# Kernel tuning notes

Measured on AMD Instinct MI355X. Metric: run time of the kernel, lower is better.

Reference implementation:

```python
import jax, jax.numpy as jnp
import numpy as np

N = 50000      # nodes
E = 800000     # edges (avg degree 16)
D = 64         # embedding_dim
G = 64         # graphs in batch
V = 30         # node label vocab (hard-coded in module)


def setup_inputs() -> dict:
    key = jax.random.key(0)
    ks = jax.random.split(key, 12)
    x = jax.random.randint(ks[0], (N,), 0, V, dtype=jnp.int32)
    edge_index = jax.random.randint(ks[1], (2, E), 0, N, dtype=jnp.int32)
    edge_attr = jax.random.uniform(ks[2], (E,), dtype=jnp.float32)
    batch = jnp.sort(jax.random.randint(ks[3], (N,), 0, G, dtype=jnp.int32))
    emb = jax.random.normal(ks[4], (V, D), dtype=jnp.float32)
    s = 1.0 / np.sqrt(D)
    W1 = jax.random.uniform(ks[5], (D, D), jnp.float32, -s, s)
    b1 = jnp.zeros((D,), jnp.float32)
    W2 = jax.random.uniform(ks[6], (D, D), jnp.float32, -s, s)
    b2 = jnp.zeros((D,), jnp.float32)
    W3 = jax.random.uniform(ks[7], (D, D), jnp.float32, -s, s)
    b3 = jnp.zeros((D,), jnp.float32)
    return {"x": x, "edge_index": edge_index, "edge_attr": edge_attr,
            "batch": batch, "emb": emb, "W1": W1, "b1": b1,
            "W2": W2, "b2": b2, "W3": W3, "b3": b3}


def _gcn(h, W, b, src, dst, norm, inv_deg):
    # GCNConv with self-loops: out_i = sum_{j->i} norm_ij * (h_j W) + (1/deg_i) * (h_i W) + b
    h = h @ W
    agg = jax.ops.segment_sum(h[src] * norm[:, None], dst, num_segments=N)
    return agg + h * inv_deg[:, None] + b


def reference(x, edge_index, edge_attr, batch, emb, W1, b1, W2, b2, W3, b3):
    src, dst = edge_index[0], edge_index[1]
    # symmetric GCN normalization with self-loops (weight 1)
    deg = jax.ops.segment_sum(edge_attr, dst, num_segments=N) + 1.0
    dis = deg ** -0.5                      # deg >= 1, so finite
    norm = dis[src] * edge_attr * dis[dst]
    inv_deg = 1.0 / deg                    # self-loop norm = dis_i * 1 * dis_i

    h = emb[x]                             # [N, D]
    h = jax.nn.relu(_gcn(h, W1, b1, src, dst, norm, inv_deg))
    h = jax.nn.relu(_gcn(h, W2, b2, src, dst, norm, inv_deg))
    h = _gcn(h, W3, b3, src, dst, norm, inv_deg)

    # global_mean_pool over graph ids
    sums = jax.ops.segment_sum(h, batch, num_segments=G)          # [G, D]
    cnts = jax.ops.segment_sum(jnp.ones((N,), h.dtype), batch, num_segments=G)
    pooled = sums / jnp.maximum(cnts, 1.0)[:, None]
    # L2 normalize rows
    nrm = jnp.linalg.norm(pooled, axis=1, keepdims=True)
    return pooled / jnp.maximum(nrm, 1e-12)
```

## Files before the change

kernel.cpp:

```cpp
#include <hip/hip_runtime.h>
#include <hip/hip_fp16.h>
#include <hip/hip_fp8.h>

#define NN 50000
#define NE 800000
#define DD 64
#define GG 64
#define VV 30
#define CAP 48
#define PBLK 512
#define PCH ((NN + PBLK - 1) / PBLK)
#define BINW 128
#define NBIN ((NN + BINW - 1) / BINW)
#define NCH 256
#define CHE ((NE + NCH - 1) / NCH)

__device__ inline unsigned char f2fp8(float f) {
    __hip_fp8_e4m3 t(f);
    return *reinterpret_cast<unsigned char*>(&t);
}
__device__ inline float fp82f(unsigned char c) {
    __hip_fp8_e4m3 t;
    *reinterpret_cast<unsigned char*>(&t) = c;
    return (float)t;
}
__device__ inline unsigned pack_edge(int s, float ea) {
    return (unsigned)s | ((unsigned)__half_as_ushort(__float2half_rn(ea)) << 16);
}
__device__ inline int unpack_src(unsigned p) { return (int)(p & 0xFFFFu); }
__device__ inline float unpack_ea(unsigned p) {
    return __half2float(__ushort_as_half((unsigned short)(p >> 16)));
}
__device__ inline unsigned short f2bf(float f) {
    unsigned u = __float_as_uint(f);
    return (unsigned short)((u + 0x7FFF + ((u >> 16) & 1)) >> 16);
}
__device__ inline float bf2f(unsigned short s) {
    return __uint_as_float(((unsigned)s) << 16);
}

__global__ __launch_bounds__(256) void k_hist(const int* __restrict__ dst,
                                              int* __restrict__ hist) {
    __shared__ int lh[NBIN];
    int t = threadIdx.x, ch = blockIdx.x;
    for (int b = t; b < NBIN; b += 256) lh[b] = 0;
    __syncthreads();
    int e0 = ch * CHE, e1 = min(e0 + CHE, NE);
    for (int e = e0 + t; e < e1; e += 256) atomicAdd(&lh[dst[e] >> 7], 1);
    __syncthreads();
    for (int b = t; b < NBIN; b += 256) hist[ch * NBIN + b] = lh[b];
}

__global__ __launch_bounds__(NCH) void k_scan_chunks(int* __restrict__ hist,
                                                     int* __restrict__ totals) {
    __shared__ int ts[NCH];
    int t = threadIdx.x, b = blockIdx.x;
    int v = hist[t * NBIN + b];
    ts[t] = v;
    __syncthreads();
    for (int off = 1; off < NCH; off <<= 1) {
        int u = (t >= off) ? ts[t - off] : 0;
        __syncthreads();
        ts[t] += u;
        __syncthreads();
    }
    hist[t * NBIN + b] = ts[t] - v;
    if (t == NCH - 1) totals[b] = ts[t];
}

__global__ __launch_bounds__(512) void k_scan_bins(const int* __restrict__ totals,
                                                   int* __restrict__ binbase) {
    __shared__ int ts[512];
    int t = threadIdx.x;
    int v = (t < NBIN) ? totals[t] : 0;
    ts[t] = v;
    __syncthreads();
    for (int off = 1; off < 512; off <<= 1) {
        int u = (t >= off) ? ts[t - off] : 0;
        __syncthreads();
        ts[t] += u;
        __syncthreads();
    }
    if (t < NBIN) binbase[t] = ts[t] - v;
    if (t == 0) binbase[NBIN] = NE;
}

__global__ __launch_bounds__(256) void k_scatter_bins(const int* __restrict__ src,
                                                      const int* __restrict__ dst,
                                                      const float* __restrict__ ea,
                                                      const int* __restrict__ hist,
                                                      const int* __restrict__ binbase,
                                                      uint2* __restrict__ sem) {
    __shared__ int lbase[NBIN];
    int t = threadIdx.x, ch = blockIdx.x;
    for (int b = t; b < NBIN; b += 256)
        lbase[b] = binbase[b] + hist[ch * NBIN + b];
    __syncthreads();
    int e0 = ch * CHE, e1 = min(e0 + CHE, NE);
    for (int e = e0 + t; e < e1; e += 256) {
        int d = dst[e];
        int p = atomicAdd(&lbase[d >> 7], 1);
        sem[p] = make_uint2(pack_edge(src[e], ea[e]), (unsigned)(d & (BINW - 1)));
    }
}

__global__ __launch_bounds__(256) void k_build(const int* __restrict__ binbase,
                                               const uint2* __restrict__ sem,
                                               unsigned* __restrict__ ep,
                                               int* __restrict__ cnt,
                                               float* __restrict__ dis) {
    __shared__ int   lcnt[BINW];
    __shared__ float lsum[BINW];
    int t = threadIdx.x, b = blockIdx.x;
    if (t < BINW) { lcnt[t] = 0; lsum[t] = 0.f; }
    __syncthreads();
    int e0 = binbase[b], e1 = binbase[b + 1];
    for (int e = e0 + t; e < e1; e += 256) {
        uint2 u = sem[e];
        int local = (int)u.y;
        int p = atomicAdd(&lcnt[local], 1);
        if (p < CAP) ep[(size_t)(b * BINW + local) * CAP + p] = u.x;
        atomicAdd(&lsum[local], unpack_ea(u.x));
    }
    __syncthreads();
    if (t < BINW) {
        int node = b * BINW + t;
        if (node < NN) {
            cnt[node] = lcnt[t];
            dis[node] = 1.0f / sqrtf(1.0f + lsum[t]);
        }
    }
}

__global__ __launch_bounds__(256) void k_emb_mm(const float* __restrict__ emb,
                                                const float* __restrict__ W,
                                                float* __restrict__ E1) {
    int t = threadIdx.x;
    int d = t & 63;
    for (int v = t >> 6; v < VV; v += 4) {
        float acc = 0.f;
        #pragma unroll
        for (int k = 0; k < 64; k++) acc = fmaf(emb[v * 64 + k], W[k * 64 + d], acc);
        E1[v * 64 + d] = acc;
    }
}

__global__ __launch_bounds__(256) void k_layer1(const int* __restrict__ cnt,
                                                const unsigned* __restrict__ ep,
                                                const float* __restrict__ dis,
                                                const int* __restrict__ x,
                                                const float* __restrict__ E1,
                                                const float* __restrict__ bias,
                                                unsigned short* __restrict__ A1) {
    __shared__ float El[VV * 64];
    int t = threadIdx.x;
    for (int i = t; i < VV * 64; i += 256) El[i] = E1[i];
    __syncthreads();
    int node = blockIdx.x * 4 + (t >> 6);
    int d = t & 63;
    if (node >= NN) return;
    int c = min(cnt[node], CAP);
    const unsigned* row = ep + (size_t)node * CAP;
    unsigned pay = (d < c) ? row[d] : 0u;
    float disn = dis[node];
    float a0 = 0.f, a1 = 0.f, a2 = 0.f, a3 = 0.f;
    int iters = (c + 7) >> 3;
    for (int it = 0; it < iters; ++it) {
        int k0 = it << 3;
        unsigned p0 = __shfl(pay, k0+0), p1 = __shfl(pay, k0+1);
        unsigned p2 = __shfl(pay, k0+2), p3 = __shfl(pay, k0+3);
        unsigned p4 = __shfl(pay, k0+4), p5 = __shfl(pay, k0+5);
        unsigned p6 = __shfl(pay, k0+6), p7 = __shfl(pay, k0+7);
        int s0 = unpack_src(p0), s1 = unpack_src(p1), s2 = unpack_src(p2), s3 = unpack_src(p3);
        int s4 = unpack_src(p4), s5 = unpack_src(p5), s6 = unpack_src(p6), s7 = unpack_src(p7);
        int x0 = x[s0], x1 = x[s1], x2 = x[s2], x3 = x[s3];
        int x4 = x[s4], x5 = x[s5], x6 = x[s6], x7 = x[s7];
        float w0 = dis[s0] * unpack_ea(p0), w1 = dis[s1] * unpack_ea(p1);
        float w2 = dis[s2] * unpack_ea(p2), w3 = dis[s3] * unpack_ea(p3);
        float w4 = dis[s4] * unpack_ea(p4), w5 = dis[s5] * unpack_ea(p5);
        float w6 = dis[s6] * unpack_ea(p6), w7 = dis[s7] * unpack_ea(p7);
        a0 = fmaf(w0, El[x0 * 64 + d], a0); a1 = fmaf(w1, El[x1 * 64 + d], a1);
        a2 = fmaf(w2, El[x2 * 64 + d], a2); a3 = fmaf(w3, El[x3 * 64 + d], a3);
        a0 = fmaf(w4, El[x4 * 64 + d], a0); a1 = fmaf(w5, El[x5 * 64 + d], a1);
        a2 = fmaf(w6, El[x6 * 64 + d], a2); a3 = fmaf(w7, El[x7 * 64 + d], a3);
    }
    float v = ((a0 + a1) + (a2 + a3)) * disn
            + El[x[node] * 64 + d] * (disn * disn) + bias[d];
    A1[(size_t)node * 64 + d] = f2bf(fmaxf(v, 0.f));
}

__global__ __launch_bounds__(256) void k_matmul(const unsigned short* __restrict__ A,
                                                const float* __restrict__ W,
                                                unsigned char* __restrict__ B) {
    __shared__ float Wl[64 * 64];
    __shared__ float Ar[16 * 64];
    int t = threadIdx.x;
    for (int i = t * 4; i < 64 * 64; i += 256 * 4)
        *(float4*)&Wl[i] = *(const float4*)&W[i];
    int q   = t & 15;
    int sub = t >> 4;
    int r0 = blockIdx.x * 64;
    for (int rg = 0; rg < 64; rg += 16) {
        __syncthreads();
        {
            int idx = t * 4;
            int rr = idx >> 6, kk = idx & 63;
            int r = r0 + rg + rr;
            float4 a = make_float4(0.f, 0.f, 0.f, 0.f);
            if (r < NN) {
                ushort4 u = *(const ushort4*)&A[(size_t)r * DD + kk];
                a = make_float4(bf2f(u.x), bf2f(u.y), bf2f(u.z), bf2f(u.w));
            }
            *(float4*)&Ar[idx] = a;
        }
        __syncthreads();
        int r = r0 + rg + sub;
        if (r < NN) {
            float4 acc = make_float4(0.f, 0.f, 0.f, 0.f);
            #pragma unroll
            for (int k = 0; k < 64; k++) {
                float a = Ar[sub * 64 + k];
                float4 w4 = *(float4*)&Wl[k * 64 + q * 4];
                acc.x = fmaf(a, w4.x, acc.x);
                acc.y = fmaf(a, w4.y, acc.y);
                acc.z = fmaf(a, w4.z, acc.z);
                acc.w = fmaf(a, w4.w, acc.w);
            }
            uchar4 o;
            o.x = f2fp8(acc.x); o.y = f2fp8(acc.y);
            o.z = f2fp8(acc.z); o.w = f2fp8(acc.w);
            *(uchar4*)&B[(size_t)r * DD + q * 4] = o;
        }
    }
}

__global__ __launch_bounds__(256) void k_spmm2(const int* __restrict__ cnt,
                                               const unsigned* __restrict__ ep,
                                               const float* __restrict__ dis,
                                               const unsigned char* __restrict__ B,
                                               const float* __restrict__ bias,
                                               unsigned char* __restrict__ A2) {
    int node = blockIdx.x * 4 + (threadIdx.x >> 6);
    int d = threadIdx.x & 63;
    if (node >= NN) return;
    int c = min(cnt[node], CAP);
    const unsigned* row = ep + (size_t)node * CAP;
    unsigned pay = (d < c) ? row[d] : 0u;
    float disn = dis[node];
    float a0 = 0.f, a1 = 0.f, a2 = 0.f, a3 = 0.f;
    int iters = (c + 7) >> 3;
    for (int it = 0; it < iters; ++it) {
        int k0 = it << 3;
        unsigned p0 = __shfl(pay, k0+0), p1 = __shfl(pay, k0+1);
        unsigned p2 = __shfl(pay, k0+2), p3 = __shfl(pay, k0+3);
        unsigned p4 = __shfl(pay, k0+4), p5 = __shfl(pay, k0+5);
        unsigned p6 = __shfl(pay, k0+6), p7 = __shfl(pay, k0+7);
        int s0 = unpack_src(p0), s1 = unpack_src(p1), s2 = unpack_src(p2), s3 = unpack_src(p3);
        int s4 = unpack_src(p4), s5 = unpack_src(p5), s6 = unpack_src(p6), s7 = unpack_src(p7);
        float g0 = fp82f(B[(size_t)s0 * 64 + d]), g1 = fp82f(B[(size_t)s1 * 64 + d]);
        float g2 = fp82f(B[(size_t)s2 * 64 + d]), g3 = fp82f(B[(size_t)s3 * 64 + d]);
        float g4 = fp82f(B[(size_t)s4 * 64 + d]), g5 = fp82f(B[(size_t)s5 * 64 + d]);
        float g6 = fp82f(B[(size_t)s6 * 64 + d]), g7 = fp82f(B[(size_t)s7 * 64 + d]);
        float w0 = dis[s0] * unpack_ea(p0), w1 = dis[s1] * unpack_ea(p1);
        float w2 = dis[s2] * unpack_ea(p2), w3 = dis[s3] * unpack_ea(p3);
        float w4 = dis[s4] * unpack_ea(p4), w5 = dis[s5] * unpack_ea(p5);
        float w6 = dis[s6] * unpack_ea(p6), w7 = dis[s7] * unpack_ea(p7);
        a0 = fmaf(w0, g0, a0); a1 = fmaf(w1, g1, a1);
        a2 = fmaf(w2, g2, a2); a3 = fmaf(w3, g3, a3);
        a0 = fmaf(w4, g4, a0); a1 = fmaf(w5, g5, a1);
        a2 = fmaf(w6, g6, a2); a3 = fmaf(w7, g7, a3);
    }
    float v = ((a0 + a1) + (a2 + a3)) * disn
            + fp82f(B[(size_t)node * 64 + d]) * (disn * disn) + bias[d];
    A2[(size_t)node * 64 + d] = f2fp8(fmaxf(v, 0.f));
}

__global__ __launch_bounds__(1024) void k_spmm3_pool(const int* __restrict__ cnt,
                                                     const unsigned* __restrict__ ep,
                                                     const float* __restrict__ dis,
                                                     const unsigned char* __restrict__ A2,
                                                     const int* __restrict__ batch,
                                                     float* __restrict__ pool,
                                                     float* __restrict__ gcnt) {
    __shared__ float lpool[GG * DD];
    __shared__ float lcnt[GG];
    int t = threadIdx.x;
    for (int i = t; i < GG * DD; i += 1024) lpool[i] = 0.f;
    if (t < GG) lcnt[t] = 0.f;
    __syncthreads();
    int base = blockIdx.x * PCH;
    int end = min(base + PCH, NN);
    int d = t & 63;
    for (int node = base + (t >> 6); node < end; node += 16) {
        int c = min(cnt[node], CAP);
        const unsigned* row = ep + (size_t)node * CAP;
        unsigned pay = (d < c) ? row[d] : 0u;
        float disn = dis[node];
        float a0 = 0.f, a1 = 0.f, a2 = 0.f, a3 = 0.f;
        int iters = (c + 7) >> 3;
        for (int it = 0; it < iters; ++it) {
            int k0 = it << 3;
            unsigned p0 = __shfl(pay, k0+0), p1 = __shfl(pay, k0+1);
            unsigned p2 = __shfl(pay, k0+2), p3 = __shfl(pay, k0+3);
            unsigned p4 = __shfl(pay, k0+4), p5 = __shfl(pay, k0+5);
            unsigned p6 = __shfl(pay, k0+6), p7 = __shfl(pay, k0+7);
            int s0 = unpack_src(p0), s1 = unpack_src(p1), s2 = unpack_src(p2), s3 = unpack_src(p3);
            int s4 = unpack_src(p4), s5 = unpack_src(p5), s6 = unpack_src(p6), s7 = unpack_src(p7);
            float g0 = fp82f(A2[(size_t)s0 * 64 + d]), g1 = fp82f(A2[(size_t)s1 * 64 + d]);
            float g2 = fp82f(A2[(size_t)s2 * 64 + d]), g3 = fp82f(A2[(size_t)s3 * 64 + d]);
            float g4 = fp82f(A2[(size_t)s4 * 64 + d]), g5 = fp82f(A2[(size_t)s5 * 64 + d]);
            float g6 = fp82f(A2[(size_t)s6 * 64 + d]), g7 = fp82f(A2[(size_t)s7 * 64 + d]);
            float w0 = dis[s0] * unpack_ea(p0), w1 = dis[s1] * unpack_ea(p1);
            float w2 = dis[s2] * unpack_ea(p2), w3 = dis[s3] * unpack_ea(p3);
            float w4 = dis[s4] * unpack_ea(p4), w5 = dis[s5] * unpack_ea(p5);
            float w6 = dis[s6] * unpack_ea(p6), w7 = dis[s7] * unpack_ea(p7);
            a0 = fmaf(w0, g0, a0); a1 = fmaf(w1, g1, a1);
            a2 = fmaf(w2, g2, a2); a3 = fmaf(w3, g3, a3);
            a0 = fmaf(w4, g4, a0); a1 = fmaf(w5, g5, a1);
            a2 = fmaf(w6, g6, a2); a3 = fmaf(w7, g7, a3);
        }
        float v = ((a0 + a1) + (a2 + a3)) * disn
                + fp82f(A2[(size_t)node * 64 + d]) * (disn * disn);
        int g = batch[node];
        atomicAdd(&lpool[g * 64 + d], v);
        if (d == 0) atomicAdd(&lcnt[g], 1.f);
    }
    __syncthreads();
    for (int i = t; i < GG * DD; i += 1024) {
        float v = lpool[i];
        if (v != 0.f) unsafeAtomicAdd(&pool[i], v);
    }
    if (t < GG) {
        float v = lcnt[t];
        if (v != 0.f) unsafeAtomicAdd(&gcnt[t], v);
    }
}

__global__ __launch_bounds__(1024) void k_final_mm(const float* __restrict__ pool,
                                                   const float* __restrict__ gcnt,
                                                   const float* __restrict__ W3,
                                                   const float* __restrict__ b3,
                                                   float* __restrict__ out) {
    __shared__ float Wl[DD * DD];
    __shared__ float Ml[GG * DD];
    int t = threadIdx.x;
    for (int i = t; i < DD * DD; i += 1024) Wl[i] = W3[i];
    for (int i = t; i < GG * DD; i += 1024) {
        int g = i >> 6;
        Ml[i] = pool[i] / fmaxf(gcnt[g], 1.0f);
    }
    __syncthreads();
    int w = t >> 6, d = t & 63;
    for (int g = w; g < GG; g += 16) {
        float acc = b3[d];
        #pragma unroll
        for (int k = 0; k < 64; k++) acc = fmaf(Ml[g * 64 + k], Wl[k * 64 + d], acc);
        float ss = acc * acc;
        #pragma unroll
        for (int o = 32; o > 0; o >>= 1) ss += __shfl_xor(ss, o);
        out[g * 64 + d] = acc / fmaxf(sqrtf(ss), 1e-12f);
    }
}

extern "C" void kernel_launch(void* const* d_in, const int* in_sizes, int n_in,
                              void* d_out, int out_size, void* d_ws, size_t ws_size,
                              hipStream_t stream) {
    const int*   x    = (const int*)d_in[0];
    const int*   ei   = (const int*)d_in[1];
    const int*   src  = ei;
    const int*   dst  = ei + NE;
    const float* ea   = (const float*)d_in[2];
    const int*   batch= (const int*)d_in[3];
    const float* emb  = (const float*)d_in[4];
    const float* Ws[3] = {(const float*)d_in[5], (const float*)d_in[7], (const float*)d_in[9]};
    const float* bs[3] = {(const float*)d_in[6], (const float*)d_in[8], (const float*)d_in[10]};
    float* out = (float*)d_out;

    char* ws = (char*)d_ws;
    size_t off = 0;
    auto alloc = [&](size_t nb) -> void* {
        void* p = ws + off;
        off = (off + nb + 255) & ~(size_t)255;
        return p;
    };
    float*          dis    = (float*)alloc((size_t)NN * 4);
    int*            cntN   = (int*)  alloc((size_t)NN * 4);
    unsigned*       ep     = (unsigned*)alloc((size_t)NBIN * BINW * CAP * 4);
    int*            hist   = (int*)  alloc((size_t)NCH * NBIN * 4);
    int*            totals = (int*)  alloc((size_t)NBIN * 4);
    int*            binbase= (int*)  alloc((size_t)(NBIN + 1) * 4);
    uint2*          sem    = (uint2*)alloc((size_t)NE * 8);
    unsigned short* A1     = (unsigned short*)alloc((size_t)NN * DD * 2);
    unsigned char*  B      = (unsigned char*)alloc((size_t)NN * DD);
    unsigned char*  A2     = (unsigned char*)alloc((size_t)NN * DD);
    float*          E1     = (float*)alloc((size_t)VV * DD * 4);
    float*          pool   = (float*)alloc((size_t)GG * DD * 4);
    float*          cnt    = (float*)alloc((size_t)GG * 4);

    k_hist<<<NCH, 256, 0, stream>>>(dst, hist);
    k_scan_chunks<<<NBIN, NCH, 0, stream>>>(hist, totals);
    k_scan_bins<<<1, 512, 0, stream>>>(totals, binbase);
    k_scatter_bins<<<NCH, 256, 0, stream>>>(src, dst, ea, hist, binbase, sem);
    k_build<<<NBIN, 256, 0, stream>>>(binbase, sem, ep, cntN, dis);

    k_emb_mm<<<1, 256, 0, stream>>>(emb, Ws[0], E1);
    k_layer1<<<(NN + 3) / 4, 256, 0, stream>>>(cntN, ep, dis, x, E1, bs[0], A1);

    k_matmul<<<(NN + 63) / 64, 256, 0, stream>>>(A1, Ws[1], B);
    k_spmm2<<<(NN + 3) / 4, 256, 0, stream>>>(cntN, ep, dis, B, bs[1], A2);

    hipMemsetAsync(pool, 0, (size_t)GG * DD * 4, stream);
    hipMemsetAsync(cnt, 0, (size_t)GG * 4, stream);
    k_spmm3_pool<<<PBLK, 1024, 0, stream>>>(cntN, ep, dis, A2, batch, pool, cnt);

    k_final_mm<<<1, 1024, 0, stream>>>(pool, cnt, Ws[2], bs[2], out);
}
```

Before: 156.4 us.

## Fuse layer-2 matmul into SpMM, fold small setup into scan, register-accumulate pooling

Layer 2 now aggregates bf16 A1 neighbours first and applies W2 afterwards inside the same kernel, using wave shuffles against an LDS copy of W2. This removes the separate matmul kernel and the fp8 intermediate buffer B. The embedding matmul and the pool/count zeroing move into the single-block scan kernel, which drops one launch and two memsets. Pooling keeps a per-thread running sum while the graph id stays the same, so it issues far fewer LDS atomics. The cost is a 64-step shuffle-FMA per node, and the gathers now read 2-byte bf16 rows instead of 1-byte fp8, roughly doubling gather traffic in layer 2.

Result: slower. 166.2 us (+6.2%).

```diff
diff --git a/kernel.cpp b/kernel.cpp
--- a/kernel.cpp
+++ b/kernel.cpp
@@ -69,7 +69,12 @@
 }
 
 __global__ __launch_bounds__(512) void k_scan_bins(const int* __restrict__ totals,
-                                                   int* __restrict__ binbase) {
+                                                   int* __restrict__ binbase,
+                                                   const float* __restrict__ emb,
+                                                   const float* __restrict__ W1,
+                                                   float* __restrict__ E1,
+                                                   float* __restrict__ pool,
+                                                   float* __restrict__ gcnt) {
     __shared__ int ts[512];
     int t = threadIdx.x;
     int v = (t < NBIN) ? totals[t] : 0;
@@ -83,6 +88,15 @@
     }
     if (t < NBIN) binbase[t] = ts[t] - v;
     if (t == 0) binbase[NBIN] = NE;
+    for (int i = t; i < VV * DD; i += 512) {
+        int vv = i >> 6, d = i & 63;
+        float acc = 0.f;
+        #pragma unroll
+        for (int k = 0; k < 64; k++) acc = fmaf(emb[vv * 64 + k], W1[k * 64 + d], acc);
+        E1[i] = acc;
+    }
+    for (int i = t; i < GG * DD; i += 512) pool[i] = 0.f;
+    if (t < GG) gcnt[t] = 0.f;
 }
 
 __global__ __launch_bounds__(256) void k_scatter_bins(const int* __restrict__ src,
@@ -129,19 +143,6 @@
             cnt[node] = lcnt[t];
             dis[node] = 1.0f / sqrtf(1.0f + lsum[t]);
         }
-    }
-}
-
-__global__ __launch_bounds__(256) void k_emb_mm(const float* __restrict__ emb,
-                                                const float* __restrict__ W,
-                                                float* __restrict__ E1) {
-    int t = threadIdx.x;
-    int d = t & 63;
-    for (int v = t >> 6; v < VV; v += 4) {
-        float acc = 0.f;
-        #pragma unroll
-        for (int k = 0; k < 64; k++) acc = fmaf(emb[v * 64 + k], W[k * 64 + d], acc);
-        E1[v * 64 + d] = acc;
     }
 }
 
@@ -189,60 +190,20 @@
     A1[(size_t)node * 64 + d] = f2bf(fmaxf(v, 0.f));
 }
 
-__global__ __launch_bounds__(256) void k_matmul(const unsigned short* __restrict__ A,
-                                                const float* __restrict__ W,
-                                                unsigned char* __restrict__ B) {
+__global__ __launch_bounds__(256) void k_layer2(const int* __restrict__ cnt,
+                                                const unsigned* __restrict__ ep,
+                                                const float* __restrict__ dis,
+                                                const unsigned short* __restrict__ A1,
+                                                const float* __restrict__ W2,
+                                                const float* __restrict__ bias,
+                                                unsigned char* __restrict__ A2) {
     __shared__ float Wl[64 * 64];
-    __shared__ float Ar[16 * 64];
     int t = threadIdx.x;
     for (int i = t * 4; i < 64 * 64; i += 256 * 4)
-        *(float4*)&Wl[i] = *(const float4*)&W[i];
-    int q   = t & 15;
-    int sub = t >> 4;
-    int r0 = blockIdx.x * 64;
-    for (int rg = 0; rg < 64; rg += 16) {
-        __syncthreads();
-        {
-            int idx = t * 4;
-            int rr = idx >> 6, kk = idx & 63;
-            int r = r0 + rg + rr;
-            float4 a = make_float4(0.f, 0.f, 0.f, 0.f);
-            if (r < NN) {
-                ushort4 u = *(const ushort4*)&A[(size_t)r * DD + kk];
-                a = make_float4(bf2f(u.x), bf2f(u.y), bf2f(u.z), bf2f(u.w));
-            }
-            *(float4*)&Ar[idx] = a;
-        }
-        __syncthreads();
-        int r = r0 + rg + sub;
-        if (r < NN) {
-            float4 acc = make_float4(0.f, 0.f, 0.f, 0.f);
-            #pragma unroll
-            for (int k = 0; k < 64; k++) {
-                float a = Ar[sub * 64 + k];
-                float4 w4 = *(float4*)&Wl[k * 64 + q * 4];
-                acc.x = fmaf(a, w4.x, acc.x);
-                acc.y = fmaf(a, w4.y, acc.y);
-                acc.z = fmaf(a, w4.z, acc.z);
-                acc.w = fmaf(a, w4.w, acc.w);
-            }
-            uchar4 o;
-            o.x = f2fp8(acc.x); o.y = f2fp8(acc.y);
-            o.z = f2fp8(acc.z); o.w = f2fp8(acc.w);
-            *(uchar4*)&B[(size_t)r * DD + q * 4] = o;
-        }
-    }
-}
-
-__global__ __launch_bounds__(256) void k_spmm2(const int* __restrict__ cnt,
-                                               const unsigned* __restrict__ ep,
-                                               const float* __restrict__ dis,
-                                               const unsigned char* __restrict__ B,
-                                               const float* __restrict__ bias,
-                                               unsigned char* __restrict__ A2) {
-    int node = blockIdx.x * 4 + (threadIdx.x >> 6);
-    int d = threadIdx.x & 63;
-    if (node >= NN) return;
+        *(float4*)&Wl[i] = *(const float4*)&W2[i];
+    __syncthreads();
+    int node = blockIdx.x * 4 + (t >> 6);
+    int d = t & 63;
     int c = min(cnt[node], CAP);
     const unsigned* row = ep + (size_t)node * CAP;
     unsigned pay = (d < c) ? row[d] : 0u;
@@ -257,10 +218,10 @@
         unsigned p6 = __shfl(pay, k0+6), p7 = __shfl(pay, k0+7);
         int s0 = unpack_src(p0), s1 = unpack_src(p1), s2 = unpack_src(p2), s3 = unpack_src(p3);
         int s4 = unpack_src(p4), s5 = unpack_src(p5), s6 = unpack_src(p6), s7 = unpack_src(p7);
-        float g0 = fp82f(B[(size_t)s0 * 64 + d]), g1 = fp82f(B[(size_t)s1 * 64 + d]);
-        float g2 = fp82f(B[(size_t)s2 * 64 + d]), g3 = fp82f(B[(size_t)s3 * 64 + d]);
-        float g4 = fp82f(B[(size_t)s4 * 64 + d]), g5 = fp82f(B[(size_t)s5 * 64 + d]);
-        float g6 = fp82f(B[(size_t)s6 * 64 + d]), g7 = fp82f(B[(size_t)s7 * 64 + d]);
+        float g0 = bf2f(A1[(size_t)s0 * 64 + d]), g1 = bf2f(A1[(size_t)s1 * 64 + d]);
+        float g2 = bf2f(A1[(size_t)s2 * 64 + d]), g3 = bf2f(A1[(size_t)s3 * 64 + d]);
+        float g4 = bf2f(A1[(size_t)s4 * 64 + d]), g5 = bf2f(A1[(size_t)s5 * 64 + d]);
+        float g6 = bf2f(A1[(size_t)s6 * 64 + d]), g7 = bf2f(A1[(size_t)s7 * 64 + d]);
         float w0 = dis[s0] * unpack_ea(p0), w1 = dis[s1] * unpack_ea(p1);
         float w2 = dis[s2] * unpack_ea(p2), w3 = dis[s3] * unpack_ea(p3);
         float w4 = dis[s4] * unpack_ea(p4), w5 = dis[s5] * unpack_ea(p5);
@@ -270,9 +231,13 @@
         a0 = fmaf(w4, g4, a0); a1 = fmaf(w5, g5, a1);
         a2 = fmaf(w6, g6, a2); a3 = fmaf(w7, g7, a3);
     }
-    float v = ((a0 + a1) + (a2 + a3)) * disn
-            + fp82f(B[(size_t)node * 64 + d]) * (disn * disn) + bias[d];
-    A2[(size_t)node * 64 + d] = f2fp8(fmaxf(v, 0.f));
+    float agg = ((a0 + a1) + (a2 + a3)) * disn
+              + bf2f(A1[(size_t)node * 64 + d]) * (disn * disn);
+    float acc = bias[d];
+    #pragma unroll
+    for (int k = 0; k < 64; k++)
+        acc = fmaf(__shfl(agg, k), Wl[k * 64 + d], acc);
+    A2[(size_t)node * 64 + d] = f2fp8(fmaxf(acc, 0.f));
 }
 
 __global__ __launch_bounds__(1024) void k_spmm3_pool(const int* __restrict__ cnt,
@@ -291,6 +256,8 @@
     int base = blockIdx.x * PCH;
     int end = min(base + PCH, NN);
     int d = t & 63;
+    int curg = -1;
+    float racc = 0.f, rcnt = 0.f;
     for (int node = base + (t >> 6); node < end; node += 16) {
         int c = min(cnt[node], CAP);
         const unsigned* row = ep + (size_t)node * CAP;
@@ -322,8 +289,18 @@
         float v = ((a0 + a1) + (a2 + a3)) * disn
                 + fp82f(A2[(size_t)node * 64 + d]) * (disn * disn);
         int g = batch[node];
-        atomicAdd(&lpool[g * 64 + d], v);
-        if (d == 0) atomicAdd(&lcnt[g], 1.f);
+        if (g != curg) {
+            if (curg >= 0) {
+                atomicAdd(&lpool[curg * 64 + d], racc);
+                if (d == 0) atomicAdd(&lcnt[curg], rcnt);
+            }
+            curg = g; racc = 0.f; rcnt = 0.f;
+        }
+        racc += v; rcnt += 1.f;
+    }
+    if (curg >= 0) {
+        atomicAdd(&lpool[curg * 64 + d], racc);
+        if (d == 0) atomicAdd(&lcnt[curg], rcnt);
     }
     __syncthreads();
     for (int i = t; i < GG * DD; i += 1024) {
@@ -391,7 +368,6 @@
     int*            binbase= (int*)  alloc((size_t)(NBIN + 1) * 4);
     uint2*          sem    = (uint2*)alloc((size_t)NE * 8);
     unsigned short* A1     = (unsigned short*)alloc((size_t)NN * DD * 2);
-    unsigned char*  B      = (unsigned char*)alloc((size_t)NN * DD);
     unsigned char*  A2     = (unsigned char*)alloc((size_t)NN * DD);
     float*          E1     = (float*)alloc((size_t)VV * DD * 4);
     float*          pool   = (float*)alloc((size_t)GG * DD * 4);
@@ -399,18 +375,14 @@
 
     k_hist<<<NCH, 256, 0, stream>>>(dst, hist);
     k_scan_chunks<<<NBIN, NCH, 0, stream>>>(hist, totals);
-    k_scan_bins<<<1, 512, 0, stream>>>(totals, binbase);
+    k_scan_bins<<<1, 512, 0, stream>>>(totals, binbase, emb, Ws[0], E1, pool, cnt);
     k_scatter_bins<<<NCH, 256, 0, stream>>>(src, dst, ea, hist, binbase, sem);
     k_build<<<NBIN, 256, 0, stream>>>(binbase, sem, ep, cntN, dis);
 
-    k_emb_mm<<<1, 256, 0, stream>>>(emb, Ws[0], E1);
     k_layer1<<<(NN + 3) / 4, 256, 0, stream>>>(cntN, ep, dis, x, E1, bs[0], A1);
 
-    k_matmul<<<(NN + 63) / 64, 256, 0, stream>>>(A1, Ws[1], B);
-    k_spmm2<<<(NN + 3) / 4, 256, 0, stream>>>(cntN, ep, dis, B, bs[1], A2);
-
-    hipMemsetAsync(pool, 0, (size_t)GG * DD * 4, stream);
-    hipMemsetAsync(cnt, 0, (size_t)GG * 4, stream);
+    k_layer2<<<NN / 4, 256, 0, stream>>>(cntN, ep, dis, A1, Ws[1], bs[1], A2);
+
     k_spmm3_pool<<<PBLK, 1024, 0, stream>>>(cntN, ep, dis, A2, batch, pool, cnt);
 
     k_final_mm<<<1, 1024, 0, stream>>>(pool, cnt, Ws[2], bs[2], out);
```
